# Optimization experiments

Measured on AMD Instinct MI355X. Metric: run time of the kernel, lower is better.

Reference implementation:

```python
import jax, jax.numpy as jnp
import numpy as np

B, C, H, W = 4, 256, 48, 48
NH = 8
HD = C // NH
SCALE = HD ** -0.5


def setup_inputs() -> dict:
    key = jax.random.key(0)
    ks = jax.random.split(key, 9)
    std = 1.0 / np.sqrt(C)
    return {
        "x": jax.random.normal(ks[0], (B, C, H, W), dtype=jnp.float32),
        "Wq": jax.random.normal(ks[1], (C, C), dtype=jnp.float32) * std,
        "bq": jax.random.normal(ks[2], (C,), dtype=jnp.float32) * std,
        "Wk": jax.random.normal(ks[3], (C, C), dtype=jnp.float32) * std,
        "bk": jax.random.normal(ks[4], (C,), dtype=jnp.float32) * std,
        "Wv": jax.random.normal(ks[5], (C, C), dtype=jnp.float32) * std,
        "bv": jax.random.normal(ks[6], (C,), dtype=jnp.float32) * std,
        "Wo": jax.random.normal(ks[7], (C, C), dtype=jnp.float32) * std,
        "bo": jax.random.normal(ks[8], (C,), dtype=jnp.float32) * std,
    }


def _proj(x, Wm, bm):
    # 1x1 conv == pointwise channel matmul; x: [B,C,H,W], Wm: [out,in]
    return jnp.einsum('bchw,oc->bohw', x, Wm) + bm[None, :, None, None]


def reference(x, Wq, bq, Wk, bk, Wv, bv, Wo, bo):
    b, c, h, w = x.shape
    s = h * w
    # [B,C,H,W] -> [B, NH, S, HD]
    def heads(t):
        return t.reshape(b, NH, HD, s).transpose(0, 1, 3, 2)
    q = heads(_proj(x, Wq, bq))
    k = heads(_proj(x, Wk, bk))
    v = heads(_proj(x, Wv, bv))
    attn = jax.nn.softmax(jnp.einsum('bhsd,bhtd->bhst', q, k) * SCALE, axis=-1)
    out = jnp.einsum('bhst,bhtd->bhsd', attn, v)
    out = out.transpose(0, 1, 3, 2).reshape(b, c, h, w)
    out = _proj(out, Wo, bo)
    return out + x
```

## Files before the change

### kernel.cpp

```cpp
#include <hip/hip_runtime.h>
#include <hip/hip_bf16.h>

#define BATCH 4
#define CCH   256
#define SS    2304
#define NHEAD 8
#define HD    32
#define SCALE_L2E (1.4426950408889634f * 0.17677669529663687f)

using bf16x8 = __attribute__((ext_vector_type(8))) short;
using v4s    = __attribute__((ext_vector_type(4))) short;
using v8s    = __attribute__((ext_vector_type(8))) short;
using f32x4  = __attribute__((ext_vector_type(4))) float;

static __device__ __forceinline__ unsigned short f2bf(float f) {
    union { float f; unsigned u; } a; a.f = f;
    unsigned r = a.u + 0x7fff + ((a.u >> 16) & 1);
    return (unsigned short)(r >> 16);
}
static __device__ __forceinline__ unsigned pk2(float a, float b) {
    return (unsigned)f2bf(a) | ((unsigned)f2bf(b) << 16);
}
static __device__ __forceinline__ v4s pack4(float a, float b, float c, float d) {
    float2 lo; lo.x = a; lo.y = b;
    float2 hi; hi.x = c; hi.y = d;
    union { __hip_bfloat162 h2[2]; v4s s; } u;
    u.h2[0] = __float22bfloat162_rn(lo);
    u.h2[1] = __float22bfloat162_rn(hi);
    return u.s;
}

__global__ __launch_bounds__(256) void wconv(const float* __restrict__ Wq, const float* __restrict__ Wk,
                                             const float* __restrict__ Wv, const float* __restrict__ Wo,
                                             unsigned short* __restrict__ wqkv, unsigned short* __restrict__ wo) {
    const int idx = blockIdx.x * 256 + threadIdx.x;
    if (idx < 768 * 256) {
        const int o = idx >> 8, c = idx & 255;
        const float v = (o < 256) ? Wq[idx] : (o < 512) ? Wk[(o - 256) * 256 + c] : Wv[(o - 512) * 256 + c];
        wqkv[idx] = f2bf(v);
    } else {
        const int j = idx - 768 * 256;
        wo[j] = f2bf(Wo[j]);
    }
}

__global__ __launch_bounds__(256) void xtrans(const float* __restrict__ x, unsigned short* __restrict__ xt) {
    __shared__ float T[64][65];
    const int b = blockIdx.z, c0 = blockIdx.y * 64, s0 = blockIdx.x * 64;
    const int tid = threadIdx.x;
    #pragma unroll
    for (int p = 0; p < 16; ++p) {
        const int c = p * 4 + (tid >> 6), s = tid & 63;
        T[c][s] = x[((size_t)(b * CCH + c0 + c)) * SS + s0 + s];
    }
    __syncthreads();
    #pragma unroll
    for (int p = 0; p < 8; ++p) {
        const int s = p * 8 + (tid >> 5), c = (tid & 31) * 2;
        *(unsigned*)&xt[((size_t)(b * SS + s0 + s)) * CCH + c0 + c] = pk2(T[c][s], T[c + 1][s]);
    }
}

__global__ __launch_bounds__(256) void gemm_qkv(const unsigned short* __restrict__ xt,
                                                const unsigned short* __restrict__ wqkv,
                                                const float* __restrict__ bq, const float* __restrict__ bk,
                                                const float* __restrict__ bv,
                                                unsigned short* __restrict__ qt, unsigned short* __restrict__ kt,
                                                unsigned short* __restrict__ vp) {
    __shared__ char Eb[4][9216];
    const int b  = blockIdx.z;
    const int o0 = blockIdx.x * 64, s0 = blockIdx.y * 128;
    const int tid = threadIdx.x, wid = tid >> 6, lane = tid & 63;
    const int lr = lane & 15, lg = lane >> 4;
    const int o_w = o0 + (wid & 1) * 32, s_w = s0 + (wid >> 1) * 64;

    const f32x4 zero4 = {0.f, 0.f, 0.f, 0.f};
    f32x4 acc[2][4];
    #pragma unroll
    for (int ai = 0; ai < 2; ++ai)
        #pragma unroll
        for (int bj = 0; bj < 4; ++bj) acc[ai][bj] = zero4;

    #pragma unroll
    for (int c0 = 0; c0 < 256; c0 += 32) {
        bf16x8 a[2], bb[4];
        #pragma unroll
        for (int ai = 0; ai < 2; ++ai)
            a[ai] = *(const bf16x8*)&wqkv[(size_t)(o_w + ai * 16 + lr) * 256 + c0 + lg * 8];
        #pragma unroll
        for (int bj = 0; bj < 4; ++bj)
            bb[bj] = *(const bf16x8*)&xt[((size_t)b * SS + s_w + bj * 16 + lr) * 256 + c0 + lg * 8];
        #pragma unroll
        for (int ai = 0; ai < 2; ++ai)
            #pragma unroll
            for (int bj = 0; bj < 4; ++bj)
                acc[ai][bj] = __builtin_amdgcn_mfma_f32_16x16x32_bf16(a[ai], bb[bj], acc[ai][bj], 0, 0, 0);
    }

    const int t = o0 >> 8;
    const int o_loc = o_w - t * 256;
    const float* bias = (t == 0) ? bq : (t == 1) ? bk : bv;

    float vals[2][4][4];
    #pragma unroll
    for (int ai = 0; ai < 2; ++ai)
        #pragma unroll
        for (int bj = 0; bj < 4; ++bj)
            #pragma unroll
            for (int i = 0; i < 4; ++i) {
                float vv = acc[ai][bj][i] + bias[o_loc + ai * 16 + 4 * lg + i];
                if (t == 0) vv *= SCALE_L2E;
                vals[ai][bj][i] = vv;
            }

    if (t < 2) {
        unsigned short* dst = (t == 0) ? qt : kt;
        unsigned short* Ls = (unsigned short*)Eb[wid];
        #pragma unroll
        for (int ai = 0; ai < 2; ++ai)
            #pragma unroll
            for (int bj = 0; bj < 4; ++bj) {
                uint2 w;
                w.x = pk2(vals[ai][bj][0], vals[ai][bj][1]);
                w.y = pk2(vals[ai][bj][2], vals[ai][bj][3]);
                *(uint2*)&Ls[(bj * 16 + lr) * 40 + ai * 16 + 4 * lg] = w;
            }
        const int h = o_loc >> 5;
        const size_t base = (size_t)(b * NHEAD + h) * SS;
        #pragma unroll
        for (int p = 0; p < 4; ++p) {
            const int cid = p * 64 + lane;
            const int s_loc = cid >> 2, oc = cid & 3;
            uint4 v = *(const uint4*)&Ls[s_loc * 40 + oc * 8];
            *(uint4*)&dst[(base + s_w + s_loc) * HD + oc * 8] = v;
        }
    } else {
        float* Lf = (float*)Eb[wid];
        #pragma unroll
        for (int ai = 0; ai < 2; ++ai)
            #pragma unroll
            for (int bj = 0; bj < 4; ++bj)
                #pragma unroll
                for (int i = 0; i < 4; ++i)
                    Lf[(ai * 16 + 4 * lg + i) * 68 + bj * 16 + lr] = vals[ai][bj][i];
        #pragma unroll
        for (int p = 0; p < 4; ++p) {
            const int cid = p * 64 + lane;
            const int oc = cid >> 3, sc8 = (cid & 7) * 8;
            float4 f0 = *(const float4*)&Lf[oc * 68 + sc8];
            float4 f1 = *(const float4*)&Lf[oc * 68 + sc8 + 4];
            uint4 w;
            w.x = pk2(f0.x, f0.y); w.y = pk2(f0.z, f0.w);
            w.z = pk2(f1.x, f1.y); w.w = pk2(f1.z, f1.w);
            *(uint4*)&vp[((size_t)(b * CCH) + o_loc + oc) * SS + s_w + sc8] = w;
        }
    }
}


#define SBAR __builtin_amdgcn_sched_barrier(0)

#define STAGE_LOAD(T0) do {                                                                \
    kreg = *(const v8s*)(ksrc + (size_t)(T0) * HD);                                        \
    vl   = *(const v4s*)(vsrc0 + (T0));                                                    \
    vh   = *(const v4s*)(vsrc1 + (T0));                                                    \
} while (0)

#define STAGE_WRITE(BUF) do {                                                              \
    *(v8s*)&Kbuf[BUF][wid * 512 + lane * 8] = kreg;                                        \
    *(v8s*)&Vbuf[BUF][wid * 512 + lane * 8] =                                              \
        __builtin_shufflevector(vl, vh, 0, 1, 2, 3, 4, 5, 6, 7);                           \
} while (0)

#define ATT_COMPUTE(BUF) do {                                                              \
    bf16x8 KF[4]; v8s VV[4];                                                               \
    _Pragma("unroll") for (int tt = 0; tt < 4; ++tt)                                       \
        KF[tt] = *(const bf16x8*)&Kbuf[BUF][tt * 512 + lane * 8];                          \
    _Pragma("unroll") for (int tt = 0; tt < 4; ++tt)                                       \
        VV[tt] = *(const v8s*)&Vbuf[BUF][tt * 512 + lane * 8];                             \
    f32x4 sc[4];                                                                           \
    _Pragma("unroll") for (int tt = 0; tt < 4; ++tt)                                       \
        sc[tt] = __builtin_amdgcn_mfma_f32_16x16x32_bf16(KF[tt], qf, zero4, 0, 0, 0);      \
    float p[16];                                                                           \
    _Pragma("unroll") for (int tt = 0; tt < 4; ++tt)                                       \
        _Pragma("unroll") for (int i = 0; i < 4; ++i)                                      \
            p[tt * 4 + i] = __builtin_amdgcn_exp2f(sc[tt][i]);                             \
    _Pragma("unroll") for (int tt = 0; tt < 4; ++tt)                                       \
        psum += (p[tt * 4] + p[tt * 4 + 1]) + (p[tt * 4 + 2] + p[tt * 4 + 3]);             \
    _Pragma("unroll") for (int tt = 0; tt < 4; ++tt) {                                     \
        const v4s pf = pack4(p[tt * 4], p[tt * 4 + 1], p[tt * 4 + 2], p[tt * 4 + 3]);      \
        const v4s v0 = __builtin_shufflevector(VV[tt], VV[tt], 0, 1, 2, 3);                \
        const v4s v1 = __builtin_shufflevector(VV[tt], VV[tt], 4, 5, 6, 7);                \
        acc[0] = __builtin_amdgcn_mfma_f32_16x16x16bf16_1k(v0, pf, acc[0], 0, 0, 0);       \
        acc[1] = __builtin_amdgcn_mfma_f32_16x16x16bf16_1k(v1, pf, acc[1], 0, 0, 0);       \
    }                                                                                      \
} while (0)

__global__ __launch_bounds__(256, 4) void attn(const unsigned short* __restrict__ qt,
                                               const unsigned short* __restrict__ kt,
                                               const unsigned short* __restrict__ vp,
                                               unsigned short* __restrict__ ot) {
    __shared__ short Kbuf[2][2048];
    __shared__ short Vbuf[2][2048];

    const int tid = threadIdx.x;
    const int wid = tid >> 6, lane = tid & 63;
    const int lr = lane & 15, lg = lane >> 4;

    const int bid = blockIdx.x;
    const int xs = bid & 7, w = bid >> 3;
    const int bh = xs * 4 + w / 36;
    const int q0 = (w % 36) * 64 + wid * 16;
    const int b  = bh >> 3, h = bh & 7;

    const unsigned short* qtb = qt + (size_t)bh * SS * HD;
    const unsigned short* ktb = kt + (size_t)bh * SS * HD;
    const unsigned short* vb  = vp + (size_t)(b * CCH + h * HD) * SS;

    const unsigned short* ksrc  = ktb + (size_t)(wid * 16 + lr) * HD + lg * 8;
    const unsigned short* vsrc0 = vb + (size_t)lr * SS + wid * 16 + lg * 4;
    const unsigned short* vsrc1 = vb + (size_t)(16 + lr) * SS + wid * 16 + lg * 4;

    const f32x4 zero4 = {0.f, 0.f, 0.f, 0.f};

    bf16x8 qf = *(const bf16x8*)&qtb[(size_t)(q0 + lr) * HD + lg * 8];

    f32x4 acc[2];
    acc[0] = zero4; acc[1] = zero4;
    float psum = 0.f;

    v8s kreg; v4s vl, vh;

    STAGE_LOAD(0);
    STAGE_WRITE(0);
    __syncthreads();

    #pragma unroll 1
    for (int ii = 0; ii < 18; ++ii) {
        STAGE_LOAD((2 * ii + 1) * 64);
        SBAR;
        ATT_COMPUTE(0);
        SBAR;
        STAGE_WRITE(1);
        __syncthreads();
        if (ii < 17) {
            STAGE_LOAD((2 * ii + 2) * 64);
        }
        SBAR;
        ATT_COMPUTE(1);
        SBAR;
        if (ii < 17) {
            STAGE_WRITE(0);
        }
        __syncthreads();
    }

    psum += __shfl_xor(psum, 16);
    psum += __shfl_xor(psum, 32);

    const float inv = 1.f / psum;
    #pragma unroll
    for (int dh = 0; dh < 2; ++dh) {
        const float o0v = acc[dh][0] * inv;
        const float o1v = acc[dh][1] * inv;
        const float o2v = acc[dh][2] * inv;
        const float o3v = acc[dh][3] * inv;
        const v4s sv = pack4(o0v, o1v, o2v, o3v);
        *(v4s*)&ot[((size_t)b * SS + q0 + lr) * CCH + h * HD + dh * 16 + 4 * lg] = sv;
    }
}

__global__ __launch_bounds__(256) void gemm_o(const unsigned short* __restrict__ ot,
                                              const unsigned short* __restrict__ wo,
                                              const float* __restrict__ bo, const float* __restrict__ x,
                                              float* __restrict__ out) {
    const int b  = blockIdx.z;
    const int o0 = blockIdx.x * 64, s0 = blockIdx.y * 128;
    const int tid = threadIdx.x, wid = tid >> 6, lane = tid & 63;
    const int lr = lane & 15, lg = lane >> 4;
    const int o_w = o0 + (wid & 1) * 32, s_w = s0 + (wid >> 1) * 64;

    const f32x4 zero4 = {0.f, 0.f, 0.f, 0.f};
    f32x4 acc[2][4];
    #pragma unroll
    for (int ai = 0; ai < 2; ++ai)
        #pragma unroll
        for (int bj = 0; bj < 4; ++bj) acc[ai][bj] = zero4;

    #pragma unroll
    for (int c0 = 0; c0 < 256; c0 += 32) {
        bf16x8 a[2], bb[4];
        #pragma unroll
        for (int ai = 0; ai < 2; ++ai)
            a[ai] = *(const bf16x8*)&wo[(size_t)(o_w + ai * 16 + lr) * 256 + c0 + lg * 8];
        #pragma unroll
        for (int bj = 0; bj < 4; ++bj)
            bb[bj] = *(const bf16x8*)&ot[((size_t)b * SS + s_w + bj * 16 + lr) * 256 + c0 + lg * 8];
        #pragma unroll
        for (int ai = 0; ai < 2; ++ai)
            #pragma unroll
            for (int bj = 0; bj < 4; ++bj)
                acc[ai][bj] = __builtin_amdgcn_mfma_f32_16x16x32_bf16(a[ai], bb[bj], acc[ai][bj], 0, 0, 0);
    }

    #pragma unroll
    for (int ai = 0; ai < 2; ++ai)
        #pragma unroll
        for (int bj = 0; bj < 4; ++bj)
            #pragma unroll
            for (int i = 0; i < 4; ++i) {
                const int o = o_w + ai * 16 + 4 * lg + i;
                const int s = s_w + bj * 16 + lr;
                const size_t idx = (size_t)(b * CCH + o) * SS + s;
                out[idx] = acc[ai][bj][i] + bo[o] + x[idx];
            }
}

extern "C" void kernel_launch(void* const* d_in, const int* in_sizes, int n_in,
                              void* d_out, int out_size, void* d_ws, size_t ws_size,
                              hipStream_t stream) {
    const float* x  = (const float*)d_in[0];
    const float* Wq = (const float*)d_in[1];
    const float* bq = (const float*)d_in[2];
    const float* Wk = (const float*)d_in[3];
    const float* bk = (const float*)d_in[4];
    const float* Wv = (const float*)d_in[5];
    const float* bv = (const float*)d_in[6];
    const float* Wo = (const float*)d_in[7];
    const float* bo = (const float*)d_in[8];
    float* out = (float*)d_out;

    const size_t plane = (size_t)BATCH * CCH * SS;
    unsigned short* xt   = (unsigned short*)d_ws;
    unsigned short* qtw  = xt  + plane;
    unsigned short* ktw  = qtw + plane;
    unsigned short* vpw  = ktw + plane;
    unsigned short* otw  = vpw + plane;
    unsigned short* wqkv = otw + plane;
    unsigned short* wob  = wqkv + 768 * 256;

    wconv<<<dim3(1024), dim3(256), 0, stream>>>(Wq, Wk, Wv, Wo, wqkv, wob);
    xtrans<<<dim3(SS / 64, CCH / 64, BATCH), dim3(256), 0, stream>>>(x, xt);
    gemm_qkv<<<dim3(12, 18, BATCH), dim3(256), 0, stream>>>(xt, wqkv, bq, bk, bv, qtw, ktw, vpw);
    attn<<<dim3(1152), dim3(256), 0, stream>>>(qtw, ktw, vpw, otw);
    gemm_o<<<dim3(4, 18, BATCH), dim3(256), 0, stream>>>(otw, wob, bo, x, out);
}
```

Measured before the change: 105.4 us.

## Merge prep kernels, shrink attention blocks, compute softmax sum via MFMA

Fuses weight conversion and the x transpose into a single prep launch, which saves one kernel launch. The attention kernel moves to 128-thread blocks with twice as many blocks, so each wave stages two K/V tiles. The row-sum of the softmax numerators is now computed by an extra MFMA against a ones vector instead of scalar adds plus cross-lane shuffles. The kernel also raises wave priority around the compute section. The cost is one extra MFMA per tile and more staging work per wave.

```diff
diff --git a/kernel.cpp b/kernel.cpp
--- a/kernel.cpp
+++ b/kernel.cpp
@@ -30,34 +30,38 @@
     return u.s;
 }
 
-__global__ __launch_bounds__(256) void wconv(const float* __restrict__ Wq, const float* __restrict__ Wk,
-                                             const float* __restrict__ Wv, const float* __restrict__ Wo,
-                                             unsigned short* __restrict__ wqkv, unsigned short* __restrict__ wo) {
-    const int idx = blockIdx.x * 256 + threadIdx.x;
-    if (idx < 768 * 256) {
-        const int o = idx >> 8, c = idx & 255;
-        const float v = (o < 256) ? Wq[idx] : (o < 512) ? Wk[(o - 256) * 256 + c] : Wv[(o - 512) * 256 + c];
-        wqkv[idx] = f2bf(v);
+__global__ __launch_bounds__(256) void prep(const float* __restrict__ Wq, const float* __restrict__ Wk,
+                                            const float* __restrict__ Wv, const float* __restrict__ Wo,
+                                            const float* __restrict__ x,
+                                            unsigned short* __restrict__ wqkv, unsigned short* __restrict__ wo,
+                                            unsigned short* __restrict__ xt) {
+    __shared__ float T[64][65];
+    const int tid = threadIdx.x;
+    if (blockIdx.x < 1024) {
+        const int idx = blockIdx.x * 256 + tid;
+        if (idx < 768 * 256) {
+            const int o = idx >> 8, c = idx & 255;
+            const float v = (o < 256) ? Wq[idx] : (o < 512) ? Wk[(o - 256) * 256 + c] : Wv[(o - 512) * 256 + c];
+            wqkv[idx] = f2bf(v);
+        } else {
+            const int j = idx - 768 * 256;
+            wo[j] = f2bf(Wo[j]);
+        }
     } else {
-        const int j = idx - 768 * 256;
-        wo[j] = f2bf(Wo[j]);
-    }
-}
-
-__global__ __launch_bounds__(256) void xtrans(const float* __restrict__ x, unsigned short* __restrict__ xt) {
-    __shared__ float T[64][65];
-    const int b = blockIdx.z, c0 = blockIdx.y * 64, s0 = blockIdx.x * 64;
-    const int tid = threadIdx.x;
-    #pragma unroll
-    for (int p = 0; p < 16; ++p) {
-        const int c = p * 4 + (tid >> 6), s = tid & 63;
-        T[c][s] = x[((size_t)(b * CCH + c0 + c)) * SS + s0 + s];
-    }
-    __syncthreads();
-    #pragma unroll
-    for (int p = 0; p < 8; ++p) {
-        const int s = p * 8 + (tid >> 5), c = (tid & 31) * 2;
-        *(unsigned*)&xt[((size_t)(b * SS + s0 + s)) * CCH + c0 + c] = pk2(T[c][s], T[c + 1][s]);
+        const int e = blockIdx.x - 1024;
+        const int b = e / 144, rem = e % 144;
+        const int c0 = (rem / 36) * 64, s0 = (rem % 36) * 64;
+        #pragma unroll
+        for (int p = 0; p < 16; ++p) {
+            const int c = p * 4 + (tid >> 6), s = tid & 63;
+            T[c][s] = x[((size_t)(b * CCH + c0 + c)) * SS + s0 + s];
+        }
+        __syncthreads();
+        #pragma unroll
+        for (int p = 0; p < 8; ++p) {
+            const int s = p * 8 + (tid >> 5), c = (tid & 31) * 2;
+            *(unsigned*)&xt[((size_t)(b * SS + s0 + s)) * CCH + c0 + c] = pk2(T[c][s], T[c + 1][s]);
+        }
     }
 }
 
@@ -161,15 +165,21 @@
 #define SBAR __builtin_amdgcn_sched_barrier(0)
 
 #define STAGE_LOAD(T0) do {                                                                \
-    kreg = *(const v8s*)(ksrc + (size_t)(T0) * HD);                                        \
-    vl   = *(const v4s*)(vsrc0 + (T0));                                                    \
-    vh   = *(const v4s*)(vsrc1 + (T0));                                                    \
+    kregA = *(const v8s*)(ksrcA + (size_t)(T0) * HD);                                      \
+    kregB = *(const v8s*)(ksrcB + (size_t)(T0) * HD);                                      \
+    vlA   = *(const v4s*)(vsrc0A + (T0));                                                  \
+    vhA   = *(const v4s*)(vsrc1A + (T0));                                                  \
+    vlB   = *(const v4s*)(vsrc0B + (T0));                                                  \
+    vhB   = *(const v4s*)(vsrc1B + (T0));                                                  \
 } while (0)
 
 #define STAGE_WRITE(BUF) do {                                                              \
-    *(v8s*)&Kbuf[BUF][wid * 512 + lane * 8] = kreg;                                        \
-    *(v8s*)&Vbuf[BUF][wid * 512 + lane * 8] =                                              \
-        __builtin_shufflevector(vl, vh, 0, 1, 2, 3, 4, 5, 6, 7);                           \
+    *(v8s*)&Kbuf[BUF][ttA * 512 + lane * 8] = kregA;                                       \
+    *(v8s*)&Kbuf[BUF][ttB * 512 + lane * 8] = kregB;                                       \
+    *(v8s*)&Vbuf[BUF][ttA * 512 + lane * 8] =                                              \
+        __builtin_shufflevector(vlA, vhA, 0, 1, 2, 3, 4, 5, 6, 7);                         \
+    *(v8s*)&Vbuf[BUF][ttB * 512 + lane * 8] =                                              \
+        __builtin_shufflevector(vlB, vhB, 0, 1, 2, 3, 4, 5, 6, 7);                         \
 } while (0)
 
 #define ATT_COMPUTE(BUF) do {                                                              \
@@ -178,6 +188,7 @@
         KF[tt] = *(const bf16x8*)&Kbuf[BUF][tt * 512 + lane * 8];                          \
     _Pragma("unroll") for (int tt = 0; tt < 4; ++tt)                                       \
         VV[tt] = *(const v8s*)&Vbuf[BUF][tt * 512 + lane * 8];                             \
+    __builtin_amdgcn_s_setprio(1);                                                         \
     f32x4 sc[4];                                                                           \
     _Pragma("unroll") for (int tt = 0; tt < 4; ++tt)                                       \
         sc[tt] = __builtin_amdgcn_mfma_f32_16x16x32_bf16(KF[tt], qf, zero4, 0, 0, 0);      \
@@ -185,18 +196,18 @@
     _Pragma("unroll") for (int tt = 0; tt < 4; ++tt)                                       \
         _Pragma("unroll") for (int i = 0; i < 4; ++i)                                      \
             p[tt * 4 + i] = __builtin_amdgcn_exp2f(sc[tt][i]);                             \
-    _Pragma("unroll") for (int tt = 0; tt < 4; ++tt)                                       \
-        psum += (p[tt * 4] + p[tt * 4 + 1]) + (p[tt * 4 + 2] + p[tt * 4 + 3]);             \
     _Pragma("unroll") for (int tt = 0; tt < 4; ++tt) {                                     \
         const v4s pf = pack4(p[tt * 4], p[tt * 4 + 1], p[tt * 4 + 2], p[tt * 4 + 3]);      \
         const v4s v0 = __builtin_shufflevector(VV[tt], VV[tt], 0, 1, 2, 3);                \
         const v4s v1 = __builtin_shufflevector(VV[tt], VV[tt], 4, 5, 6, 7);                \
         acc[0] = __builtin_amdgcn_mfma_f32_16x16x16bf16_1k(v0, pf, acc[0], 0, 0, 0);       \
         acc[1] = __builtin_amdgcn_mfma_f32_16x16x16bf16_1k(v1, pf, acc[1], 0, 0, 0);       \
+        accP   = __builtin_amdgcn_mfma_f32_16x16x16bf16_1k(vOnes, pf, accP, 0, 0, 0);      \
     }                                                                                      \
+    __builtin_amdgcn_s_setprio(0);                                                         \
 } while (0)
 
-__global__ __launch_bounds__(256, 4) void attn(const unsigned short* __restrict__ qt,
+__global__ __launch_bounds__(128, 4) void attn(const unsigned short* __restrict__ qt,
                                                const unsigned short* __restrict__ kt,
                                                const unsigned short* __restrict__ vp,
                                                unsigned short* __restrict__ ot) {
@@ -209,27 +220,32 @@
 
     const int bid = blockIdx.x;
     const int xs = bid & 7, w = bid >> 3;
-    const int bh = xs * 4 + w / 36;
-    const int q0 = (w % 36) * 64 + wid * 16;
+    const int bh = xs * 4 + w / 72;
+    const int q0 = (w % 72) * 32 + wid * 16;
     const int b  = bh >> 3, h = bh & 7;
 
     const unsigned short* qtb = qt + (size_t)bh * SS * HD;
     const unsigned short* ktb = kt + (size_t)bh * SS * HD;
     const unsigned short* vb  = vp + (size_t)(b * CCH + h * HD) * SS;
 
-    const unsigned short* ksrc  = ktb + (size_t)(wid * 16 + lr) * HD + lg * 8;
-    const unsigned short* vsrc0 = vb + (size_t)lr * SS + wid * 16 + lg * 4;
-    const unsigned short* vsrc1 = vb + (size_t)(16 + lr) * SS + wid * 16 + lg * 4;
+    const int ttA = wid * 2, ttB = wid * 2 + 1;
+    const unsigned short* ksrcA  = ktb + (size_t)(ttA * 16 + lr) * HD + lg * 8;
+    const unsigned short* ksrcB  = ktb + (size_t)(ttB * 16 + lr) * HD + lg * 8;
+    const unsigned short* vsrc0A = vb + (size_t)lr * SS + ttA * 16 + lg * 4;
+    const unsigned short* vsrc1A = vb + (size_t)(16 + lr) * SS + ttA * 16 + lg * 4;
+    const unsigned short* vsrc0B = vb + (size_t)lr * SS + ttB * 16 + lg * 4;
+    const unsigned short* vsrc1B = vb + (size_t)(16 + lr) * SS + ttB * 16 + lg * 4;
 
     const f32x4 zero4 = {0.f, 0.f, 0.f, 0.f};
+    const v4s vOnes = {(short)0x3F80, (short)0x3F80, (short)0x3F80, (short)0x3F80};
 
     bf16x8 qf = *(const bf16x8*)&qtb[(size_t)(q0 + lr) * HD + lg * 8];
 
     f32x4 acc[2];
     acc[0] = zero4; acc[1] = zero4;
-    float psum = 0.f;
-
-    v8s kreg; v4s vl, vh;
+    f32x4 accP = zero4;
+
+    v8s kregA, kregB; v4s vlA, vhA, vlB, vhB;
 
     STAGE_LOAD(0);
     STAGE_WRITE(0);
@@ -255,10 +271,7 @@
         __syncthreads();
     }
 
-    psum += __shfl_xor(psum, 16);
-    psum += __shfl_xor(psum, 32);
-
-    const float inv = 1.f / psum;
+    const float inv = 1.f / accP[0];
     #pragma unroll
     for (int dh = 0; dh < 2; ++dh) {
         const float o0v = acc[dh][0] * inv;
@@ -339,9 +352,8 @@
     unsigned short* wqkv = otw + plane;
     unsigned short* wob  = wqkv + 768 * 256;
 
-    wconv<<<dim3(1024), dim3(256), 0, stream>>>(Wq, Wk, Wv, Wo, wqkv, wob);
-    xtrans<<<dim3(SS / 64, CCH / 64, BATCH), dim3(256), 0, stream>>>(x, xt);
+    prep<<<dim3(1600), dim3(256), 0, stream>>>(Wq, Wk, Wv, Wo, x, wqkv, wob, xt);
     gemm_qkv<<<dim3(12, 18, BATCH), dim3(256), 0, stream>>>(xt, wqkv, bq, bk, bv, qtw, ktw, vpw);
-    attn<<<dim3(1152), dim3(256), 0, stream>>>(qtw, ktw, vpw, otw);
+    attn<<<dim3(2304), dim3(128), 0, stream>>>(qtw, ktw, vpw, otw);
     gemm_o<<<dim3(4, 18, BATCH), dim3(256), 0, stream>>>(otw, wob, bo, x, out);
 }
```

Measured after the change: 142.6 us. +35.3%, slower.
